# Kernel tuning notes

Hardware: AMD Instinct MI355X
Metric: run time of the kernel (lower is better)

The kernel has to match this reference:

```python
import jax, jax.numpy as jnp
import numpy as np

N, E = 32768, 262144
IN_C, OUT_C = 128, 128
N_GRAPHS = 64


def setup_inputs() -> dict:
    key = jax.random.key(0)
    ks = jax.random.split(key, 8)
    x = jax.random.normal(ks[0], (N, IN_C), dtype=jnp.float32)
    edge_index = jax.random.randint(ks[1], (2, E), 0, N, dtype=jnp.int32)
    batch = jnp.sort(jax.random.randint(ks[2], (N,), 0, N_GRAPHS, dtype=jnp.int32))
    rand = jax.random.uniform(ks[3], (E,), dtype=jnp.float32)  # replaces random.random() draws
    lim_t = 1.0 / np.sqrt(IN_C)
    W_t = jax.random.uniform(ks[4], (IN_C, OUT_C), jnp.float32, -lim_t, lim_t)
    b_t = jax.random.uniform(ks[5], (OUT_C,), jnp.float32, -lim_t, lim_t)
    lim_s = 1.0 / np.sqrt(OUT_C)
    W_s = jax.random.uniform(ks[6], (OUT_C, 1), jnp.float32, -lim_s, lim_s)
    b_s = jax.random.uniform(ks[7], (1,), jnp.float32, -lim_s, lim_s)
    return dict(x=x, edge_index=edge_index, batch=batch, rand=rand,
                W_t=W_t, b_t=b_t, W_s=W_s, b_s=b_s)


def _greedy_match(scores, src, dst, rand, n):
    """Sequential greedy edge matching over score-sorted edges.
    Returns (order, cid_sorted, n_merged): cid_sorted[i] is the cluster id
    assigned to sorted edge i, or -1 if rejected/skipped."""
    scores = jax.lax.stop_gradient(scores)  # indices are non-differentiable (torch uses .item())
    rand = jax.lax.stop_gradient(rand)
    order = jnp.argsort(-scores)
    s_o, d_o = src[order], dst[order]
    acc = rand[order] <= scores[order]  # torch: skip edge if r > edge_score

    def step(carry, inp):
        avail, nxt = carry
        s, t, a = inp
        ok = a & avail[s] & avail[t]
        cid = jnp.where(ok, nxt, -1)
        avail = avail.at[s].set(avail[s] & ~ok)
        avail = avail.at[t].set(avail[t] & ~ok)
        return (avail, nxt + ok.astype(jnp.int32)), cid

    (_, n_merged), cid_sorted = jax.lax.scan(
        step, (jnp.ones((n,), bool), jnp.int32(0)), (s_o, d_o, acc))
    return order, cid_sorted, n_merged


def reference(x, edge_index, batch, rand, W_t, b_t, W_s, b_s):
    n = x.shape[0]
    src, dst = edge_index[0], edge_index[1]
    # merge_edge_sum + transform (eval mode, dropout p=0)
    x_merged = (x[src] + x[dst]) @ W_t + b_t          # [E, OUT_C]
    x_self = (x + x) @ W_t + b_t                      # [N, OUT_C] (self-edge merge)
    e = jax.nn.sigmoid((x_merged @ W_s).reshape(-1) + b_s[0])  # [E] edge scores

    order, cid_sorted, n_merged = _greedy_match(e, src, dst, rand, n)
    ok = cid_sorted >= 0                              # accepted sorted edges
    s_o, d_o = src[order], dst[order]

    # node -> cluster assignment (sentinel index n is dropped)
    cluster = jnp.full((n,), -1, jnp.int32)
    cluster = cluster.at[jnp.where(ok, s_o, n)].set(cid_sorted, mode='drop')
    cluster = cluster.at[jnp.where(ok, d_o, n)].set(cid_sorted, mode='drop')
    remaining = cluster < 0
    rem_rank = jnp.cumsum(remaining.astype(jnp.int32)) - 1  # ascending node order, like set iteration
    cluster = jnp.where(remaining, n_merged + rem_rank, cluster)
    num_clusters = n_merged + remaining.sum().astype(jnp.int32)

    # pooled features, padded to [n, OUT_C]; rows [0, num_clusters) are valid
    mcid = jnp.where(ok, cid_sorted, n)
    new_x = jnp.zeros((n, x_merged.shape[1]), x.dtype)
    new_x = new_x.at[mcid].set(x_merged[order], mode='drop')
    new_x = new_x.at[jnp.where(remaining, cluster, n)].set(x_self, mode='drop')

    # per-cluster edge score (1.0 for unmerged singleton nodes)
    new_edge_score = jnp.ones((n,), e.dtype).at[mcid].set(e[order], mode='drop')

    # new batch vector: new_batch[cluster[v]] = batch[v]
    new_batch = jnp.zeros((n,), batch.dtype).at[cluster].set(batch)

    # remapped edges + coalesce/remove_self_loops expressed as a validity mask
    new_ei = cluster[edge_index]                      # [2, E]
    key = new_ei[0].astype(jnp.int64) * n + new_ei[1].astype(jnp.int64)
    perm = jnp.argsort(key)
    ksorted = key[perm]
    first = jnp.concatenate([jnp.array([True]), ksorted[1:] != ksorted[:-1]])
    unique = jnp.zeros((key.shape[0],), bool).at[perm].set(first)
    edge_valid = unique & (new_ei[0] != new_ei[1])

    return new_x, cluster, new_batch, new_edge_score, num_clusters, new_ei, edge_valid, e
```

## Files before the change

### kernel.cpp

```cpp
#include <hip/hip_runtime.h>
#include <stdint.h>

typedef unsigned int u32;
typedef unsigned long long u64;

#define NN 32768
#define NE 262144
#define NC 128

#define O0 0u
#define O1 4194304u
#define O2 4227072u
#define O3 4259840u
#define O4 4292608u
#define O5 4292609u
#define O6 4816897u
#define O7 5079041u

#define HCAP (1u<<19)
#define NFULL 8
#define CNT0 8
#define MCAP 16384
#define SCAP 32768
#define SNB 32
#define MAXK 0xFFFFFFFFFFFFFFFFull
#define PREFLAG (1ull<<62)

__global__ void ep_init(const float* Wt, const float* Ws, const float* bt, const float* bs,
                        double* u, double* c0, u32* counters,
                        u64* b0, u64* b1, u32* avail, int* cl,
                        u32* tkey, u32* tmin, u32* histA) {
    u32 i = blockIdx.x*blockDim.x + threadIdx.x;
    if (blockIdx.x == 0 && threadIdx.x < 128) {
        int r = threadIdx.x;
        double s = 0.0;
        for (int j = 0; j < NC; j++) s += (double)Wt[r*NC+j] * (double)Ws[j];
        u[r] = s;
        if (r == 0) {
            double c = 0.0;
            for (int j = 0; j < NC; j++) c += (double)bt[j] * (double)Ws[j];
            *c0 = c + (double)bs[0];
        }
    }
    if (i < 64) counters[i] = 0u;
    if (i < NN) { b0[i] = MAXK; b1[i] = MAXK; cl[i] = -1; }
    if (i < NN/32) avail[i] = 0xFFFFFFFFu;
    if (i < 8192) histA[i] = 0u;
    for (u32 j = i; j < HCAP; j += 131072u) { tkey[j] = 0xFFFFFFFFu; tmin[j] = 0xFFFFFFFFu; }
}

__global__ void ep_ynode(const float* x, const double* u, double* y) {
    int gid = blockIdx.x*blockDim.x + threadIdx.x;
    int v = gid >> 6, lane = threadIdx.x & 63;
    if (v >= NN) return;
    double t = (double)x[v*NC+lane]*u[lane] + (double)x[v*NC+lane+64]*u[lane+64];
    for (int off = 32; off; off >>= 1) t += __shfl_down(t, off, 64);
    if (lane == 0) y[v] = t;
}

__global__ void ep_escore(const int* src, const int* dst, const float* rnd, const double* y,
                          const double* c0, u64* fkey, u64* fdat, u32* counters, float* out) {
    int e = blockIdx.x*blockDim.x + threadIdx.x;
    if (e >= NE) return;
    int s = src[e], d = dst[e];
    double z = y[s] + y[d] + *c0;
    double sc = 1.0/(1.0 + exp(-z));
    out[O7 + e] = (float)sc;
    u64 b = (u64)__double_as_longlong(z);
    u64 ord = (b & 0x8000000000000000ull) ? ~b : (b | 0x8000000000000000ull);
    u64 P = ((~ord) & 0xFFFFFFFFFFFC0000ull) | (u64)(u32)e;
    if ((double)rnd[e] <= sc) {
        u32 p = atomicAdd(&counters[CNT0], 1u);
        fkey[p] = P;
        fdat[p] = ((u64)(u32)e << 30) | ((u64)(u32)s << 15) | (u64)(u32)d;
    }
}

__device__ __forceinline__ bool ep_bit(const u32* a, u32 v) { return (a[v>>5] >> (v&31)) & 1u; }

__global__ void ep_rA(const u64* fkey, const u64* fdat, const u32* cnt, u64* bt, const u32* avail) {
    u32 n = *cnt;
    for (u32 i = blockIdx.x*blockDim.x + threadIdx.x; i < n; i += 131072u) {
        u64 v = fdat[i];
        u32 s = (u32)((v>>15)&0x7FFF), d = (u32)(v&0x7FFF);
        if (ep_bit(avail, s) && ep_bit(avail, d)) {
            u64 P = fkey[i];
            atomicMin(&bt[s], P); atomicMin(&bt[d], P);
        }
    }
}

__global__ void ep_rB(const u64* fkey, const u64* fdat, const u32* cnt, u32* cntN,
                      u64* fkeyN, u64* fdatN, const u64* bt, u64* btN, u32* avail,
                      u64* mkey, u64* mpay, u32* counters) {
    u32 n = *cnt;
    for (u32 i = blockIdx.x*blockDim.x + threadIdx.x; i < n; i += 131072u) {
        u64 v = fdat[i];
        u32 s = (u32)((v>>15)&0x7FFF), d = (u32)(v&0x7FFF);
        if (!ep_bit(avail, s) || !ep_bit(avail, d)) continue;
        u64 P = fkey[i];
        if (bt[s] == P && bt[d] == P) {
            u32 slot = atomicAdd(&counters[2], 1u);
            mkey[slot] = P; mpay[slot] = v;
            atomicAnd(&avail[s>>5], ~(1u<<(s&31)));
            atomicAnd(&avail[d>>5], ~(1u<<(d&31)));
        } else {
            u32 p = atomicAdd(cntN, 1u);
            fkeyN[p] = P; fdatN[p] = v;
            btN[s] = MAXK; btN[d] = MAXK;
        }
    }
}

__global__ void ep_merge(const u64* mk, const u64* mp, const u64* fk, const u64* fd,
                         u32* counters, u64* ck, u64* cd2, u32* hist) {
    u32 i = blockIdx.x*blockDim.x + threadIdx.x;
    u32 nm0 = counters[2];
    u32 cr  = counters[CNT0+NFULL];
    u32 tot = nm0 + cr; if (tot > SCAP) tot = SCAP;
    if (i == 0) counters[4] = tot;
    u64 K = MAXK, D = 0;
    if (i < nm0) { K = mk[i]; D = mp[i] | PREFLAG; }
    else if (i < tot) { K = fk[i-nm0]; D = fd[i-nm0]; }
    ck[i] = K; cd2[i] = D;
    if (i < tot) atomicAdd(&hist[((u32)(K >> 16) & 255u)*SNB + (i>>10)], 1u);
}

__global__ void ms_scan(u32* hist, u32* histNext) {
    int t = threadIdx.x;
    int per = 256*SNB/64;
    int base = t*per;
    u32 s = 0;
    for (int j = 0; j < per; j++) s += hist[base+j];
    u32 x = s;
    for (int off = 1; off < 64; off <<= 1) { u32 yv = __shfl_up(x, off, 64); if (t >= off) x += yv; }
    u32 run = x - s;
    for (int j = 0; j < per; j++) { u32 tmp = hist[base+j]; hist[base+j] = run; run += tmp; }
    if (histNext) { for (int j = t; j < 8192; j += 64) histNext[j] = 0u; }
}

__global__ void ms_scat(const u64* ki, const u64* pi, u64* ko, u64* po,
                        const u32* hist, int shift, const u32* counters, u32* histNext) {
    __shared__ unsigned short m[256][64];
    int t = threadIdx.x;
    u32 cnt = counters[4];
    for (int i = t; i < 8192; i += 64) ((u32*)m)[i] = 0u;
    __syncthreads();
    u32 base = blockIdx.x*1024u + (u32)t*16u;
    u64 kr[16]; u32 dg[16];
    #pragma unroll
    for (u32 j = 0; j < 16; j++) {
        bool real = (base+j < cnt);
        kr[j] = real ? ki[base+j] : MAXK;
        dg[j] = (u32)(kr[j] >> shift) & 255u;
        if (real) m[dg[j]][t]++;
    }
    __syncthreads();
    for (int k = 0; k < 4; k++) {
        int d = t*4 + k;
        u32 run = 0;
        for (int tt = 0; tt < 64; tt++) { u32 tmp = m[d][tt]; m[d][tt] = (unsigned short)run; run += tmp; }
    }
    __syncthreads();
    #pragma unroll
    for (u32 j = 0; j < 16; j++) {
        if (base+j < cnt) {
            u32 d = dg[j];
            u32 pos = hist[d*SNB + blockIdx.x] + m[d][t];
            m[d][t]++;
            ko[pos] = kr[j];
            po[pos] = pi[base+j];
            if (histNext) atomicAdd(&histNext[((u32)(kr[j] >> (shift+8)) & 255u)*SNB + (pos>>10)], 1u);
        }
    }
}

__global__ void ep_csum(const u64* sd, const u32* counters, u32* mflag, u32* csums) {
    u32 i = blockIdx.x*1024 + threadIdx.x;
    u32 cnt = counters[4];
    u64 v = sd[i];
    bool pre = (i < cnt) && ((v & PREFLAG) != 0);
    bool cand = (i < cnt) && !pre;
    mflag[i] = pre ? 1u : 0u;
    int c = __syncthreads_count(cand ? 1 : 0);
    if (threadIdx.x == 0) csums[blockIdx.x] = (u32)c;
}

__global__ void ep_cscan(u32* csums, u32* counters, int which) {
    int t = threadIdx.x;
    u32 v = (t < SNB) ? csums[t] : 0u;
    u32 x = v;
    for (int off = 1; off < 64; off <<= 1) { u32 y = __shfl_up(x, off, 64); if (t >= off) x += y; }
    if (t < SNB) csums[t] = x - v;
    if (t == SNB-1) counters[which] = x;
}

__global__ void ep_cemit(const u64* sd, const u32* counters, const u32* csums, u32* candIdx) {
    __shared__ u32 w[16];
    int t = threadIdx.x;
    u32 i = blockIdx.x*1024 + t;
    u32 cnt = counters[4];
    u64 v = sd[i];
    bool pre = (i < cnt) && ((v & PREFLAG) != 0);
    u32 c = ((i < cnt) && !pre) ? 1u : 0u;
    u32 x = c;
    for (int off = 1; off < 64; off <<= 1) { u32 y = __shfl_up(x, off, 64); if ((t&63) >= off) x += y; }
    if ((t&63) == 63) w[t>>6] = x;
    __syncthreads();
    if (t < 16) {
        u32 ww = w[t];
        for (int off = 1; off < 16; off <<= 1) { u32 y = __shfl_up(ww, off, 16); if (t >= off) ww += y; }
        w[t] = ww;
    }
    __syncthreads();
    u32 excl = ((t>>6) ? w[(t>>6)-1] : 0u) + x - c;
    if (c) candIdx[csums[blockIdx.x] + excl] = i;
}

__global__ void __launch_bounds__(1024) ep_walk(const u64* sd, const u32* candIdx,
                                                u32* counters, const u32* availG,
                                                u32* mflag, u32* msums) {
    __shared__ u32 avail[1024];
    __shared__ u32 claim[16384];
    __shared__ u32 part[1024];
    __shared__ u32 segs[32];
    int t = threadIdx.x;
    avail[t] = availG[t];
    for (int j = t; j < 16384; j += 1024) claim[j] = 0xFFFFFFFFu;
    __syncthreads();
    u32 ncand = counters[5];
    u32 iterTag = 0x3FFFFFu;
    for (u32 base = 0; base < ncand; base += 1024) {
        u32 j = base + (u32)t;
        bool have = j < ncand;
        u32 i = 0, s = 0, d = 0;
        if (have) {
            i = candIdx[j];
            u64 v = sd[i];
            s = (u32)((v>>15)&0x7FFF); d = (u32)(v&0x7FFF);
        }
        u32 hs = s & 16383u, hd = d & 16383u;
        int st = 1;
        if (have && ((avail[s>>5]>>(s&31))&1u) && ((avail[d>>5]>>(d&31))&1u)) st = 0;
        for (int guard = 0; guard < 2048; guard++) {
            u32 tag = (iterTag << 10) | (u32)t;
            if (st == 0) { atomicMin(&claim[hs], tag); atomicMin(&claim[hd], tag); }
            __syncthreads();
            if (st == 0) {
                bool aok = ((avail[s>>5]>>(s&31))&1u) && ((avail[d>>5]>>(d&31))&1u);
                if (!aok) st = 1;
                else if (claim[hs] == tag && claim[hd] == tag) {
                    st = 2;
                    atomicAnd(&avail[s>>5], ~(1u<<(s&31)));
                    atomicAnd(&avail[d>>5], ~(1u<<(d&31)));
                    mflag[i] = 1u;
                }
            }
            iterTag--;
            if (__syncthreads_count(st == 0) == 0) break;
        }
    }
    __syncthreads();
    u32 p = 0; int b2 = t*32;
    for (int j = 0; j < 32; j++) p += mflag[b2+j];
    part[t] = p;
    __syncthreads();
    if (t < 32) { u32 sg = 0; for (int j = 0; j < 32; j++) sg += part[t*32+j]; segs[t] = sg; }
    __syncthreads();
    if (t == 0) { u32 a = 0; for (int g = 0; g < 32; g++) { msums[g] = a; a += segs[g]; } counters[2] = a; }
}

__global__ void ep_memit(const u64* sd, const u32* mflag, const u32* msums,
                         const int* batch, u64* Mlist, int* cl, float* out) {
    __shared__ u32 w[16];
    int t = threadIdx.x;
    u32 i = blockIdx.x*1024 + t;
    u32 m = mflag[i];
    u32 x = m;
    for (int off = 1; off < 64; off <<= 1) { u32 y = __shfl_up(x, off, 64); if ((t&63) >= off) x += y; }
    if ((t&63) == 63) w[t>>6] = x;
    __syncthreads();
    if (t < 16) {
        u32 ww = w[t];
        for (int off = 1; off < 16; off <<= 1) { u32 y = __shfl_up(ww, off, 16); if (t >= off) ww += y; }
        w[t] = ww;
    }
    __syncthreads();
    u32 excl = ((t>>6) ? w[(t>>6)-1] : 0u) + x - m;
    if (m) {
        u32 cid = msums[blockIdx.x] + excl;
        u64 v = sd[i] & ~PREFLAG;
        u32 e = (u32)(v>>30), s = (u32)((v>>15)&0x7FFF), d = (u32)(v&0x7FFF);
        Mlist[cid] = v;
        cl[s] = (int)cid; cl[d] = (int)cid;
        u32 mx = s > d ? s : d;
        out[O2 + cid] = (float)batch[mx];
        out[O3 + cid] = out[O7 + e];
    }
}

__global__ void ep_scanN(int* cl, u32* counters, u32* slist, float* out) {
    __shared__ u32 w[16];
    int t = threadIdx.x;
    int base = t*32;
    u32 s = 0;
    for (int j = 0; j < 32; j++) s += (cl[base+j] < 0) ? 1u : 0u;
    u32 x = s;
    for (int off = 1; off < 64; off <<= 1) { u32 y = __shfl_up(x, off, 64); if ((t&63) >= off) x += y; }
    if ((t&63) == 63) w[t>>6] = x;
    __syncthreads();
    if (t < 16) {
        u32 ww = w[t];
        for (int off = 1; off < 16; off <<= 1) { u32 y = __shfl_up(ww, off, 16); if (t >= off) ww += y; }
        w[t] = ww;
    }
    __syncthreads();
    u32 excl = ((t>>6) ? w[(t>>6)-1] : 0u) + x - s;
    u32 total = w[15];
    u32 nm = counters[2];
    if (t == 0) {
        counters[3] = nm + total;
        counters[6] = total;
        out[O4] = (float)(nm + total);
    }
    u32 run = nm + excl;
    for (int j = 0; j < 32; j++) {
        if (cl[base+j] < 0) {
            slist[run - nm] = (u32)(base + j);
            cl[base+j] = (int)(run++);
        }
    }
}

__global__ void ep_out_nodes(const int* cl, const int* batch, const u32* counters, float* out) {
    int v = blockIdx.x*blockDim.x + threadIdx.x;
    if (v >= NN) return;
    u32 nm = counters[2], ncl = counters[3];
    int c = cl[v];
    out[O1 + v] = (float)c;
    if (c >= (int)nm) out[O2 + c] = (float)batch[v];
    if (v >= (int)nm) out[O3 + v] = 1.0f;
    if (v >= (int)ncl) out[O2 + v] = 0.0f;
}

__global__ void ep_newx_m(const float* x, const float* Wt, const float* bt,
                          const u64* Mlist, const u32* counters, float* out) {
    __shared__ u64 ml[32];
    __shared__ float m[32][128];
    u32 nm = counters[2];
    u32 base = blockIdx.x * 32u;
    if (base >= nm) return;
    int t = threadIdx.x, lane = t & 63, wv = t >> 6;
    if (t < 32) { u32 r = base + (u32)t; ml[t] = (r < nm) ? Mlist[r] : 0ull; }
    __syncthreads();
    for (int i = t; i < 4096; i += 256) {
        int r = i >> 7, k = i & 127;
        u64 v = ml[r];
        u32 s = (u32)((v>>15)&0x7FFF), d = (u32)(v&0x7FFF);
        m[r][k] = x[s*NC+k] + x[d*NC+k];
    }
    __syncthreads();
    float a0[8], a1[8];
    #pragma unroll
    for (int r = 0; r < 8; r++) { a0[r] = bt[lane]; a1[r] = bt[lane+64]; }
    for (int k = 0; k < 128; k++) {
        float w0 = Wt[k*NC+lane], w1 = Wt[k*NC+lane+64];
        #pragma unroll
        for (int r = 0; r < 8; r++) { float mm = m[wv*8+r][k]; a0[r] += mm*w0; a1[r] += mm*w1; }
    }
    #pragma unroll
    for (int r = 0; r < 8; r++) {
        u32 row = base + (u32)(wv*8 + r);
        if (row < nm) {
            out[O0 + (size_t)row*NC + lane]      = a0[r];
            out[O0 + (size_t)row*NC + lane + 64] = a1[r];
        }
    }
}

__global__ void ep_newx_s(const float* x, const float* Wt, const float* bt,
                          const u32* slist, const u32* counters, float* out) {
    __shared__ u32 nodes[32];
    __shared__ float m[32][128];
    u32 nm = counters[2], ncl = counters[3], sc = counters[6];
    u32 base = nm + blockIdx.x * 32u;
    if (base >= NN) return;
    int t = threadIdx.x, lane = t & 63, wv = t >> 6;
    if (base >= ncl) {
        for (int i = t; i < 4096; i += 256) {
            u32 row = base + (u32)(i >> 7);
            if (row < NN) out[O0 + (size_t)row*NC + (i & 127)] = 0.0f;
        }
        return;
    }
    if (t < 32) { u32 p = base - nm + (u32)t; nodes[t] = (p < sc) ? slist[p] : slist[0]; }
    __syncthreads();
    for (int i = t; i < 4096; i += 256) {
        int r = i >> 7, k = i & 127;
        m[r][k] = 2.0f * x[nodes[r]*NC + k];
    }
    __syncthreads();
    float a0[8], a1[8];
    #pragma unroll
    for (int r = 0; r < 8; r++) { a0[r] = bt[lane]; a1[r] = bt[lane+64]; }
    for (int k = 0; k < 128; k++) {
        float w0 = Wt[k*NC+lane], w1 = Wt[k*NC+lane+64];
        #pragma unroll
        for (int r = 0; r < 8; r++) { float mm = m[wv*8+r][k]; a0[r] += mm*w0; a1[r] += mm*w1; }
    }
    #pragma unroll
    for (int r = 0; r < 8; r++) {
        u32 row = base + (u32)(wv*8 + r);
        if (row >= NN) continue;
        if (row < ncl) {
            out[O0 + (size_t)row*NC + lane]      = a0[r];
            out[O0 + (size_t)row*NC + lane + 64] = a1[r];
        } else {
            out[O0 + (size_t)row*NC + lane]      = 0.0f;
            out[O0 + (size_t)row*NC + lane + 64] = 0.0f;
        }
    }
}

__global__ void ep_newei(const int* src, const int* dst, const int* cl,
                         u32* tkey, u32* tmin, u32* eslot, float* out) {
    int e = blockIdx.x*blockDim.x + threadIdx.x;
    if (e >= NE) return;
    u32 cs = (u32)cl[src[e]], cd = (u32)cl[dst[e]];
    out[O5 + e]      = (float)cs;
    out[O5 + NE + e] = (float)cd;
    u32 key = (cs << 15) | cd;
    u32 slot = ((key * 2654435761u) >> 11) & (HCAP-1);
    while (true) {
        u32 k = tkey[slot];
        if (k == key) break;
        if (k == 0xFFFFFFFFu) {
            u32 old = atomicCAS(&tkey[slot], 0xFFFFFFFFu, key);
            if (old == 0xFFFFFFFFu || old == key) break;
        }
        slot = (slot + 1) & (HCAP-1);
    }
    eslot[e] = slot | ((cs != cd) ? 0x80000000u : 0u);
    atomicMin(&tmin[slot], (u32)e);
}

__global__ void ep_valid(const u32* tmin, const u32* eslot, float* out) {
    int e = blockIdx.x*blockDim.x + threadIdx.x;
    if (e >= NE) return;
    u32 sl = eslot[e];
    bool valid = (tmin[sl & 0x7FFFFFFFu] == (u32)e) && (sl >> 31);
    out[O6 + e] = valid ? 1.0f : 0.0f;
}

extern "C" void kernel_launch(void* const* d_in, const int* in_sizes, int n_in,
                              void* d_out, int out_size, void* d_ws, size_t ws_size,
                              hipStream_t stream) {
    (void)in_sizes; (void)n_in; (void)out_size; (void)ws_size;
    const float* x    = (const float*)d_in[0];
    const int*   ei   = (const int*)d_in[1];
    const int*   src  = ei;
    const int*   dst  = ei + NE;
    const int*   batch= (const int*)d_in[2];
    const float* rnd  = (const float*)d_in[3];
    const float* Wt   = (const float*)d_in[4];
    const float* bt   = (const float*)d_in[5];
    const float* Ws   = (const float*)d_in[6];
    const float* bs   = (const float*)d_in[7];
    float* out = (float*)d_out;

    char* w = (char*)d_ws;
    double* u  = (double*)w;
    double* c0 = (double*)(w + 1024);
    u32* counters = (u32*)(w + 2048);
    size_t off = 4096;
    double* y   = (double*)(w + off); off += (size_t)NN*8;
    u64* fkeyA  = (u64*)(w + off); off += (size_t)NE*8;
    u64* fdatA  = (u64*)(w + off); off += (size_t)NE*8;
    u64* fkeyB  = (u64*)(w + off); off += (size_t)NE*8;
    u64* fdatB  = (u64*)(w + off); off += (size_t)NE*8;
    u64* mkeyA  = (u64*)(w + off); off += (size_t)MCAP*8;
    u64* mpayA  = (u64*)(w + off); off += (size_t)MCAP*8;
    u64* combK  = (u64*)(w + off); off += (size_t)SCAP*8;
    u64* combD  = (u64*)(w + off); off += (size_t)SCAP*8;
    u64* combK2 = (u64*)(w + off); off += (size_t)SCAP*8;
    u64* combD2 = (u64*)(w + off); off += (size_t)SCAP*8;
    u64* bt0    = (u64*)(w + off); off += (size_t)NN*8;
    u64* bt1    = (u64*)(w + off); off += (size_t)NN*8;
    u32* avail  = (u32*)(w + off); off += NN/8;
    int* cl     = (int*)(w + off); off += (size_t)NN*4;
    u64* Mlist  = (u64*)(w + off); off += (size_t)NN*8;
    u32* histA  = (u32*)(w + off); off += 8192*4;
    u32* histB  = (u32*)(w + off); off += 8192*4;
    u32* mflag  = (u32*)(w + off); off += (size_t)SCAP*4;
    u32* candIdx= (u32*)(w + off); off += (size_t)SCAP*4;
    u32* csums  = (u32*)(w + off); off += 64*4;
    u32* msums  = (u32*)(w + off); off += 64*4;
    u32* slist  = (u32*)(w + off); off += (size_t)NN*4;
    u32* tkey   = (u32*)(w + off); off += (size_t)HCAP*4;
    u32* tmin   = (u32*)(w + off); off += (size_t)HCAP*4;
    u32* eslot  = (u32*)(w + off); off += (size_t)NE*4;

    ep_init<<<512, 256, 0, stream>>>(Wt, Ws, bt, bs, u, c0, counters,
                                     bt0, bt1, avail, cl, tkey, tmin, histA);
    ep_ynode<<<8192, 256, 0, stream>>>(x, u, y);
    ep_escore<<<1024, 256, 0, stream>>>(src, dst, rnd, y, c0, fkeyA, fdatA, counters, out);

    u64 *fk = fkeyA, *fd = fdatA, *fk2 = fkeyB, *fd2 = fdatB;
    u64 *bc = bt0, *bn = bt1;
    for (u32 rd = 0; rd < NFULL; rd++) {
        ep_rA<<<512, 256, 0, stream>>>(fk, fd, &counters[CNT0+rd], bc, avail);
        ep_rB<<<512, 256, 0, stream>>>(fk, fd, &counters[CNT0+rd], &counters[CNT0+rd+1],
                                       fk2, fd2, bc, bn, avail, mkeyA, mpayA, counters);
        u64* tp;
        tp = fk; fk = fk2; fk2 = tp;
        tp = fd; fd = fd2; fd2 = tp;
        tp = bc; bc = bn; bn = tp;
    }

    ep_merge<<<SNB, 1024, 0, stream>>>(mkeyA, mpayA, fk, fd, counters, combK, combD, histA);
    u32* H[2] = {histA, histB};
    u64 *ki = combK, *pi = combD, *ko = combK2, *po = combD2;
    for (int p = 0; p < 6; p++) {
        u32* hn = (p < 5) ? H[(p+1)&1] : (u32*)nullptr;
        ms_scan<<<1, 64, 0, stream>>>(H[p&1], hn);
        ms_scat<<<SNB, 64, 0, stream>>>(ki, pi, ko, po, H[p&1], 16 + p*8, counters, hn);
        u64* tp;
        tp = ki; ki = ko; ko = tp;
        tp = pi; pi = po; po = tp;
    }

    ep_csum<<<SNB, 1024, 0, stream>>>(combD, counters, mflag, csums);
    ep_cscan<<<1, 64, 0, stream>>>(csums, counters, 5);
    ep_cemit<<<SNB, 1024, 0, stream>>>(combD, counters, csums, candIdx);
    ep_walk<<<1, 1024, 0, stream>>>(combD, candIdx, counters, avail, mflag, msums);
    ep_memit<<<SNB, 1024, 0, stream>>>(combD, mflag, msums, batch, Mlist, cl, out);

    ep_scanN<<<1, 1024, 0, stream>>>(cl, counters, slist, out);
    ep_out_nodes<<<128, 256, 0, stream>>>(cl, batch, counters, out);

    ep_newx_m<<<512, 256, 0, stream>>>(x, Wt, bt, Mlist, counters, out);
    ep_newx_s<<<1024, 256, 0, stream>>>(x, Wt, bt, slist, counters, out);

    ep_newei<<<1024, 256, 0, stream>>>(src, dst, cl, tkey, tmin, eslot, out);
    ep_valid<<<1024, 256, 0, stream>>>(tmin, eslot, out);
}
```

Before: 723.6 us.

## Restructure radix sort passes with per-block histogram kernel and wave-ballot ranking

Replaces the fused histogram-via-global-atomics and the per-thread shared-memory 256x64 counter scan in the radix scatter with a separate per-pass histogram kernel plus ballot-based peer matching. Each wave computes rank within matching digits using ballots, and a leader updates a 256-entry shared counter. This drops the serial per-digit prefix over 64 threads and the global atomics, at the cost of six extra kernel launches and an extra key read per pass. Processing order also changes from 16 contiguous elements per thread to strided per-wave chunks, which keeps the scatter stable.

```diff
diff --git a/kernel.cpp b/kernel.cpp
--- a/kernel.cpp
+++ b/kernel.cpp
@@ -29,7 +29,7 @@
 __global__ void ep_init(const float* Wt, const float* Ws, const float* bt, const float* bs,
                         double* u, double* c0, u32* counters,
                         u64* b0, u64* b1, u32* avail, int* cl,
-                        u32* tkey, u32* tmin, u32* histA) {
+                        u32* tkey, u32* tmin) {
     u32 i = blockIdx.x*blockDim.x + threadIdx.x;
     if (blockIdx.x == 0 && threadIdx.x < 128) {
         int r = threadIdx.x;
@@ -45,7 +45,6 @@
     if (i < 64) counters[i] = 0u;
     if (i < NN) { b0[i] = MAXK; b1[i] = MAXK; cl[i] = -1; }
     if (i < NN/32) avail[i] = 0xFFFFFFFFu;
-    if (i < 8192) histA[i] = 0u;
     for (u32 j = i; j < HCAP; j += 131072u) { tkey[j] = 0xFFFFFFFFu; tmin[j] = 0xFFFFFFFFu; }
 }
 
@@ -113,20 +112,48 @@
 }
 
 __global__ void ep_merge(const u64* mk, const u64* mp, const u64* fk, const u64* fd,
-                         u32* counters, u64* ck, u64* cd2, u32* hist) {
+                         u32* counters, u64* ck, u64* cd2) {
     u32 i = blockIdx.x*blockDim.x + threadIdx.x;
     u32 nm0 = counters[2];
     u32 cr  = counters[CNT0+NFULL];
-    u32 tot = nm0 + cr; if (tot > SCAP) tot = SCAP;
-    if (i == 0) counters[4] = tot;
+    if (i == 0) { u32 tot = nm0 + cr; counters[4] = tot > SCAP ? SCAP : tot; }
     u64 K = MAXK, D = 0;
     if (i < nm0) { K = mk[i]; D = mp[i] | PREFLAG; }
-    else if (i < tot) { K = fk[i-nm0]; D = fd[i-nm0]; }
+    else if (i < nm0 + cr && i < SCAP) { K = fk[i-nm0]; D = fd[i-nm0]; }
     ck[i] = K; cd2[i] = D;
-    if (i < tot) atomicAdd(&hist[((u32)(K >> 16) & 255u)*SNB + (i>>10)], 1u);
-}
-
-__global__ void ms_scan(u32* hist, u32* histNext) {
+}
+
+__device__ __forceinline__ u64 ep_peers(u32 d, bool real) {
+    u64 m = ~0ull;
+    #pragma unroll
+    for (int b = 0; b < 8; b++) {
+        u64 bb = __ballot((d >> b) & 1u);
+        m &= ((d >> b) & 1u) ? bb : ~bb;
+    }
+    return m & __ballot(real);
+}
+
+__global__ void ms_hist(const u64* key, u32* hist, int shift, const u32* counters) {
+    __shared__ u32 h[256];
+    int t = threadIdx.x;
+    u32 total = counters[4];
+    h[t] = 0; h[t+64] = 0; h[t+128] = 0; h[t+192] = 0;
+    u32 blk = blockIdx.x;
+    for (int j = 0; j < 16; j++) {
+        u32 idx = blk*1024u + (u32)j*64u + (u32)t;
+        bool real = idx < total;
+        u64 k = real ? key[idx] : MAXK;
+        u32 d = (u32)(k >> shift) & 255u;
+        u64 m = ep_peers(d, real);
+        if (real && t == (__ffsll((unsigned long long)m) - 1)) h[d] += (u32)__popcll(m);
+    }
+    hist[(u32)t*SNB + blk]       = h[t];
+    hist[((u32)t+64)*SNB + blk]  = h[t+64];
+    hist[((u32)t+128)*SNB + blk] = h[t+128];
+    hist[((u32)t+192)*SNB + blk] = h[t+192];
+}
+
+__global__ void ms_scan(u32* hist) {
     int t = threadIdx.x;
     int per = 256*SNB/64;
     int base = t*per;
@@ -136,41 +163,30 @@
     for (int off = 1; off < 64; off <<= 1) { u32 yv = __shfl_up(x, off, 64); if (t >= off) x += yv; }
     u32 run = x - s;
     for (int j = 0; j < per; j++) { u32 tmp = hist[base+j]; hist[base+j] = run; run += tmp; }
-    if (histNext) { for (int j = t; j < 8192; j += 64) histNext[j] = 0u; }
 }
 
 __global__ void ms_scat(const u64* ki, const u64* pi, u64* ko, u64* po,
-                        const u32* hist, int shift, const u32* counters, u32* histNext) {
-    __shared__ unsigned short m[256][64];
-    int t = threadIdx.x;
-    u32 cnt = counters[4];
-    for (int i = t; i < 8192; i += 64) ((u32*)m)[i] = 0u;
-    __syncthreads();
-    u32 base = blockIdx.x*1024u + (u32)t*16u;
-    u64 kr[16]; u32 dg[16];
-    #pragma unroll
-    for (u32 j = 0; j < 16; j++) {
-        bool real = (base+j < cnt);
-        kr[j] = real ? ki[base+j] : MAXK;
-        dg[j] = (u32)(kr[j] >> shift) & 255u;
-        if (real) m[dg[j]][t]++;
-    }
-    __syncthreads();
-    for (int k = 0; k < 4; k++) {
-        int d = t*4 + k;
-        u32 run = 0;
-        for (int tt = 0; tt < 64; tt++) { u32 tmp = m[d][tt]; m[d][tt] = (unsigned short)run; run += tmp; }
-    }
-    __syncthreads();
-    #pragma unroll
-    for (u32 j = 0; j < 16; j++) {
-        if (base+j < cnt) {
-            u32 d = dg[j];
-            u32 pos = hist[d*SNB + blockIdx.x] + m[d][t];
-            m[d][t]++;
-            ko[pos] = kr[j];
-            po[pos] = pi[base+j];
-            if (histNext) atomicAdd(&histNext[((u32)(kr[j] >> (shift+8)) & 255u)*SNB + (pos>>10)], 1u);
+                        const u32* hist, int shift, const u32* counters) {
+    __shared__ u32 cnt[256];
+    int t = threadIdx.x;
+    u32 total = counters[4];
+    cnt[t] = 0; cnt[t+64] = 0; cnt[t+128] = 0; cnt[t+192] = 0;
+    u32 blk = blockIdx.x;
+    for (int j = 0; j < 16; j++) {
+        u32 idx = blk*1024u + (u32)j*64u + (u32)t;
+        bool real = idx < total;
+        u64 k = real ? ki[idx] : MAXK;
+        u32 d = (u32)(k >> shift) & 255u;
+        u64 m = ep_peers(d, real);
+        if (real) {
+            u32 rank = (u32)__popcll(m & (((u64)1 << t) - 1ull));
+            int leader = __ffsll((unsigned long long)m) - 1;
+            u32 base = 0;
+            if (t == leader) { base = cnt[d]; cnt[d] = base + (u32)__popcll(m); }
+            base = __shfl(base, leader, 64);
+            u32 pos = hist[d*SNB + blk] + base + rank;
+            ko[pos] = k;
+            po[pos] = pi[idx];
         }
     }
 }
@@ -489,8 +505,7 @@
     u32* avail  = (u32*)(w + off); off += NN/8;
     int* cl     = (int*)(w + off); off += (size_t)NN*4;
     u64* Mlist  = (u64*)(w + off); off += (size_t)NN*8;
-    u32* histA  = (u32*)(w + off); off += 8192*4;
-    u32* histB  = (u32*)(w + off); off += 8192*4;
+    u32* hist   = (u32*)(w + off); off += 8192*4;
     u32* mflag  = (u32*)(w + off); off += (size_t)SCAP*4;
     u32* candIdx= (u32*)(w + off); off += (size_t)SCAP*4;
     u32* csums  = (u32*)(w + off); off += 64*4;
@@ -501,7 +516,7 @@
     u32* eslot  = (u32*)(w + off); off += (size_t)NE*4;
 
     ep_init<<<512, 256, 0, stream>>>(Wt, Ws, bt, bs, u, c0, counters,
-                                     bt0, bt1, avail, cl, tkey, tmin, histA);
+                                     bt0, bt1, avail, cl, tkey, tmin);
     ep_ynode<<<8192, 256, 0, stream>>>(x, u, y);
     ep_escore<<<1024, 256, 0, stream>>>(src, dst, rnd, y, c0, fkeyA, fdatA, counters, out);
 
@@ -517,13 +532,13 @@
         tp = bc; bc = bn; bn = tp;
     }
 
-    ep_merge<<<SNB, 1024, 0, stream>>>(mkeyA, mpayA, fk, fd, counters, combK, combD, histA);
-    u32* H[2] = {histA, histB};
+    ep_merge<<<SNB, 1024, 0, stream>>>(mkeyA, mpayA, fk, fd, counters, combK, combD);
     u64 *ki = combK, *pi = combD, *ko = combK2, *po = combD2;
     for (int p = 0; p < 6; p++) {
-        u32* hn = (p < 5) ? H[(p+1)&1] : (u32*)nullptr;
-        ms_scan<<<1, 64, 0, stream>>>(H[p&1], hn);
-        ms_scat<<<SNB, 64, 0, stream>>>(ki, pi, ko, po, H[p&1], 16 + p*8, counters, hn);
+        int shift = 16 + p*8;
+        ms_hist<<<SNB, 64, 0, stream>>>(ki, hist, shift, counters);
+        ms_scan<<<1, 64, 0, stream>>>(hist);
+        ms_scat<<<SNB, 64, 0, stream>>>(ki, pi, ko, po, hist, shift, counters);
         u64* tp;
         tp = ki; ki = ko; ko = tp;
         tp = pi; pi = po; po = tp;
```

Measured after the change: 689.5 us. -4.7%, faster.
